# Performance work log

Measured on AMD Instinct MI355X. Metric: run time of the kernel, lower is better.

Reference implementation:

```python
import jax, jax.numpy as jnp
import numpy as np

MG = (5, 5)          # mesh_grid_size
UP = (17, 17)        # upsample_size
IMG = (512.0, 512.0) # image_size
B = 8192
FC_OUT = MG[0] * MG[1] * 2  # 50
KH = (UP[0] - 1) // (MG[0] - 1) + 1  # 5
KW = (UP[1] - 1) // (MG[1] - 1) + 1  # 5
SH = (UP[0] - 1) // (MG[0] - 1)      # 4
SW = (UP[1] - 1) // (MG[1] - 1)      # 4
L0 = MG[0] - 1
L1 = MG[1] - 1


def _grid(h, w):
    # channel 0: x coords vary along rows (image_size[0]); channel 1: y along cols
    x_t = jnp.broadcast_to(jnp.linspace(0.0, IMG[0], h)[:, None], (h, w))
    y_t = jnp.broadcast_to(jnp.linspace(0.0, IMG[1], w)[None, :], (h, w))
    return jnp.stack([x_t, y_t], 0)  # [2, h, w]


def _unfold22(a):
    # a: [B, 2, H, W] -> [B, (H-1)*(W-1), 4, 2]; 4 = kernel positions row-major, 2 = channel
    p = jnp.stack([a[:, :, :-1, :-1], a[:, :, :-1, 1:],
                   a[:, :, 1:, :-1], a[:, :, 1:, 1:]], axis=2)  # [B,2,4,H-1,W-1]
    return p.reshape(a.shape[0], 2, 4, -1).transpose(0, 3, 2, 1)


def _persp(src, dst):
    # exact 4-point homography solve (torchgeometry.get_perspective_transform)
    x0, y0 = src[..., 0], src[..., 1]
    u, v = dst[..., 0], dst[..., 1]
    z = jnp.zeros_like(x0)
    o = jnp.ones_like(x0)
    ax = jnp.stack([x0, y0, o, z, z, z, -u * x0, -u * y0], -1)  # [N,4,8]
    ay = jnp.stack([z, z, z, x0, y0, o, -v * x0, -v * y0], -1)
    A = jnp.concatenate([ax, ay], 1)                 # [N,8,8]
    bb = jnp.concatenate([u, v], 1)[..., None]       # [N,8,1]
    h = jnp.linalg.solve(A, bb)[..., 0]              # [N,8]
    return jnp.concatenate([h, o[:, :1]], 1).reshape(-1, 3, 3)


def setup_inputs() -> dict:
    key = jax.random.key(0)
    ks = jax.random.split(key, 4)
    def lin(k, i, o):
        return jax.random.normal(k, (i, o), jnp.float32) / jnp.sqrt(i)
    return {
        "x": jax.random.normal(ks[0], (B, 1024), jnp.float32),
        "W1": lin(ks[1], 1024, 1024), "b1": jnp.zeros((1024,), jnp.float32),
        "W2": lin(ks[2], 1024, 2048), "b2": jnp.zeros((2048,), jnp.float32),
        "W3": lin(ks[3], 2048, FC_OUT), "b3": jnp.zeros((FC_OUT,), jnp.float32),
    }


def reference(x, W1, b1, W2, b2, W3, b3):
    Bn = x.shape[0]
    h = jax.nn.relu(x @ W1 + b1)
    h = jax.nn.relu(h @ W2 + b2)
    out = (h @ W3 + b3).reshape(Bn, 2, MG[0], MG[1])  # [B,2,5,5] mesh flow

    # sparse control grid and 2x2 patch corner points
    gs = _grid(MG[0], MG[1])
    src = _unfold22(jnp.broadcast_to(gs[None], (Bn, 2, MG[0], MG[1]))).reshape(-1, 4, 2)
    flow = _unfold22(out).reshape(-1, 4, 2)
    M = _persp(src, src + flow)  # [B*16, 3, 3]

    # dense grid and its unfold2 (kernel KHxKW, stride SHxSW) patch points
    gd = _grid(UP[0], UP[1])  # [2, 17, 17]
    gi = (np.arange(L0) * SH)[:, None, None, None] + np.arange(KH)[None, None, :, None]
    gj = (np.arange(L1) * SW)[None, :, None, None] + np.arange(KW)[None, None, None, :]
    I, J = np.broadcast_arrays(gi, gj)  # [L0,L1,KH,KW]
    pts = gd[:, I, J].transpose(1, 2, 3, 4, 0).reshape(1, L0 * L1, KH * KW, 2)
    pts = jnp.broadcast_to(pts, (Bn, L0 * L1, KH * KW, 2)).reshape(Bn * L0 * L1, KH * KW, 2)

    # transform_points: homogeneous warp + perspective divide
    ph = jnp.concatenate([pts, jnp.ones(pts.shape[:-1] + (1,), pts.dtype)], -1)
    oh = jnp.einsum('nij,npj->npi', M, ph)
    warped = oh[..., :2] / oh[..., 2:3]
    warped = warped.reshape(Bn, L0, L1, KH, KW, 2)

    # Fold: scatter-accumulate overlapping patches
    fold = jnp.zeros((Bn, 2, UP[0], UP[1]), x.dtype)
    for i in range(L0):
        for j in range(L1):
            blk = warped[:, i, j].transpose(0, 3, 1, 2)  # [B,2,KH,KW]
            fold = fold.at[:, :, i * SH:i * SH + KH, j * SW:j * SW + KW].add(blk)

    # boundary rescaling exactly as the torch code: only the 5x5 crossing points
    idx = np.arange(0, UP[0], MG[0] - 1)
    X, Y = np.meshgrid(idx, idx, indexing='xy')
    fold = fold.at[:, :, X, Y].multiply(0.5)
    for (a, b) in ((0, 0), (0, UP[1] - 1), (UP[0] - 1, UP[1] - 1), (UP[0] - 1, 0)):
        fold = fold.at[:, :, a, b].multiply(2.0)

    return fold - gd[None]  # upsampled mesh flow [B,2,17,17]
```

## Files before the change

### kernel.cpp

```cpp
#include <hip/hip_runtime.h>

typedef __bf16 bf16x8 __attribute__((ext_vector_type(8)));
typedef float f32x4 __attribute__((ext_vector_type(4)));

__device__ __forceinline__ unsigned short f2bf(float f) {
  unsigned int u = __builtin_bit_cast(unsigned int, f);
  unsigned int r = (u + 0x7fffu + ((u >> 16) & 1u)) >> 16;
  return (unsigned short)r;
}

__device__ __forceinline__ float bf2f(unsigned short u) {
  unsigned int v = ((unsigned int)u) << 16;
  return __builtin_bit_cast(float, v);
}

__device__ __forceinline__ void load16_lds(const unsigned short* g, unsigned short* l) {
  __builtin_amdgcn_global_load_lds(
      (const __attribute__((address_space(1))) void*)g,
      (__attribute__((address_space(3))) void*)l, 16, 0, 0);
}

__device__ __forceinline__ void wait_vm0() {
  asm volatile("s_waitcnt vmcnt(0)" ::: "memory");
  __builtin_amdgcn_sched_barrier(0);
}
__device__ __forceinline__ void barrier_raw() {
  __builtin_amdgcn_sched_barrier(0);
  __builtin_amdgcn_s_barrier();
  __builtin_amdgcn_sched_barrier(0);
}


__global__ __launch_bounds__(256) void prepass(
    const float* __restrict__ x, const float* __restrict__ W1,
    const float* __restrict__ W2, const float* __restrict__ W3,
    unsigned short* __restrict__ xbf, unsigned short* __restrict__ w1t,
    unsigned short* __restrict__ w2t, unsigned short* __restrict__ w3t) {
  __shared__ float tile[32][33];
  const int bid = blockIdx.x;
  const int t = threadIdx.x;
  if (bid < 2048) {
    for (int i = bid * 256 + t; i < 2097152; i += 2048 * 256) {
      float4 f = ((const float4*)x)[i];
      uint2 o;
      o.x = (unsigned)f2bf(f.x) | ((unsigned)f2bf(f.y) << 16);
      o.y = (unsigned)f2bf(f.z) | ((unsigned)f2bf(f.w) << 16);
      ((uint2*)xbf)[i] = o;
    }
  } else if (bid < 3072) {
    int ti = bid - 2048;
    int n0 = (ti & 31) * 32, k0 = (ti >> 5) * 32;
    int tx = t & 31, ty = t >> 5;
    #pragma unroll
    for (int r = 0; r < 32; r += 8)
      tile[ty + r][tx] = W1[(size_t)(k0 + ty + r) * 1024 + n0 + tx];
    __syncthreads();
    #pragma unroll
    for (int r = 0; r < 32; r += 8)
      w1t[(size_t)(n0 + ty + r) * 1024 + k0 + tx] = f2bf(tile[tx][ty + r]);
  } else if (bid < 5120) {
    int ti = bid - 3072;
    int n0 = (ti & 63) * 32, k0 = (ti >> 6) * 32;
    int tx = t & 31, ty = t >> 5;
    #pragma unroll
    for (int r = 0; r < 32; r += 8)
      tile[ty + r][tx] = W2[(size_t)(k0 + ty + r) * 2048 + n0 + tx];
    __syncthreads();
    #pragma unroll
    for (int r = 0; r < 32; r += 8)
      w2t[(size_t)(n0 + ty + r) * 1024 + k0 + tx] = f2bf(tile[tx][ty + r]);
  } else {
    int idx = (bid - 5120) * 256 + t;
    int n = idx >> 11, k = idx & 2047;
    w3t[idx] = f2bf((n < 50) ? W3[(size_t)k * 50 + n] : 0.f);
  }
}


__global__ __launch_bounds__(512, 2) void gemm1_8p(
    const unsigned short* __restrict__ A,
    const unsigned short* __restrict__ Bt,
    const float* __restrict__ bias,
    unsigned short* __restrict__ C) {
  constexpr int K = 1024, N = 1024, NT = 16;
  constexpr int AEL = 256 * 64;
  constexpr int BEL = 128 * 64;
  constexpr int BUF = AEL + BEL;
  __shared__ __align__(16) unsigned short smem[2 * BUF];
  const int t = threadIdx.x;
  const int m0 = blockIdx.x * 256;
  const int n0 = blockIdx.y * 128;
  const int lane = t & 63, wv = t >> 6;
  const int l16 = lane & 15, quad = lane >> 4;
  const int rb = (wv >> 1) * 64, cb = (wv & 1) * 64;

  const int srow = t >> 3;
  const int sg = ((t & 7) ^ (srow & 7)) * 8;
  const unsigned short* Ag0 = A + (size_t)(m0 + srow) * K + sg;
  const unsigned short* Bg0 = Bt + (size_t)(n0 + srow) * K + sg;
  const int ldsO = wv * 8 * 64;

  f32x4 acc[4][4] = {};

  #pragma unroll
  for (int r = 0; r < 4; ++r)
    load16_lds(Ag0 + (size_t)(r * 64) * K, &smem[r * 4096 + ldsO]);
  #pragma unroll
  for (int r = 0; r < 2; ++r)
    load16_lds(Bg0 + (size_t)(r * 64) * K, &smem[AEL + r * 4096 + ldsO]);

  for (int kt = 0; kt < NT; ++kt) {
    unsigned short* Ls = &smem[(kt & 1) * BUF];

    wait_vm0();
    barrier_raw();

    if (kt + 1 < NT) {
      unsigned short* Ln = &smem[((kt + 1) & 1) * BUF];
      const unsigned short* An = Ag0 + (size_t)(kt + 1) * 64;
      const unsigned short* Bn = Bg0 + (size_t)(kt + 1) * 64;
      #pragma unroll
      for (int r = 0; r < 4; ++r)
        load16_lds(An + (size_t)(r * 64) * K, &Ln[r * 4096 + ldsO]);
      #pragma unroll
      for (int r = 0; r < 2; ++r)
        load16_lds(Bn + (size_t)(r * 64) * K, &Ln[AEL + r * 4096 + ldsO]);
    }

    #pragma unroll
    for (int half = 0; half < 2; ++half) {
      bf16x8 af[4], bfr[4];
      #pragma unroll
      for (int ni = 0; ni < 4; ++ni) {
        int row = cb + ni * 16 + l16;
        bfr[ni] = *(const bf16x8*)&Ls[AEL + row * 64 + ((half * 4 + quad) ^ (row & 7)) * 8];
      }
      #pragma unroll
      for (int mi = 0; mi < 4; ++mi) {
        int row = rb + mi * 16 + l16;
        af[mi] = *(const bf16x8*)&Ls[row * 64 + ((half * 4 + quad) ^ (row & 7)) * 8];
      }
      #pragma unroll
      for (int mi = 0; mi < 4; ++mi)
        #pragma unroll
        for (int ni = 0; ni < 4; ++ni)
          acc[mi][ni] = __builtin_amdgcn_mfma_f32_16x16x32_bf16(
              af[mi], bfr[ni], acc[mi][ni], 0, 0, 0);
    }
  }
  barrier_raw();

  unsigned short* Cs = smem;
  float bv[4];
  #pragma unroll
  for (int ni = 0; ni < 4; ++ni) bv[ni] = bias[n0 + cb + ni * 16 + l16];
  #pragma unroll
  for (int mi = 0; mi < 4; ++mi)
    #pragma unroll
    for (int ni = 0; ni < 4; ++ni)
      #pragma unroll
      for (int r = 0; r < 4; ++r) {
        int row = rb + mi * 16 + quad * 4 + r;
        int col = cb + ni * 16 + l16;
        int pb = (col >> 3) ^ (row & 15);
        Cs[row * 128 + pb * 8 + (col & 7)] = f2bf(fmaxf(acc[mi][ni][r] + bv[ni], 0.f));
      }
  __syncthreads();
  #pragma unroll
  for (int j = 0; j < 8; ++j) {
    int idx = j * 512 + t;
    int row = idx >> 4, cg = idx & 15;
    int pb = cg ^ (row & 15);
    *(uint4*)&C[(size_t)(m0 + row) * N + n0 + cg * 8] =
        *(const uint4*)&Cs[row * 128 + pb * 8];
  }
}


__global__ __launch_bounds__(512, 2) void gemm2_8p(
    const unsigned short* __restrict__ A,
    const unsigned short* __restrict__ Bt,
    const float* __restrict__ bias,
    const unsigned short* __restrict__ W3t,
    unsigned short* __restrict__ part) {
  constexpr int K = 1024, NT = 16;
  constexpr int AEL = 256 * 64;
  constexpr int BUF = 2 * AEL;
  __shared__ __align__(16) unsigned short smem[2 * BUF];
  const int t = threadIdx.x;
  const int m0 = blockIdx.x * 256;
  const int n0 = blockIdx.y * 256;
  const int lane = t & 63, wv = t >> 6;
  const int l16 = lane & 15, quad = lane >> 4;
  const int rb = (wv >> 2) * 128, cb = (wv & 3) * 64;

  const int srow = t >> 3;
  const int sg = ((t & 7) ^ (srow & 7)) * 8;
  const unsigned short* Ag0 = A + (size_t)(m0 + srow) * K + sg;
  const unsigned short* Bg0 = Bt + (size_t)(n0 + srow) * K + sg;
  const int ldsO = wv * 8 * 64;

  f32x4 acc[8][4] = {};

  #pragma unroll
  for (int r = 0; r < 4; ++r) {
    load16_lds(Ag0 + (size_t)(r * 64) * K, &smem[r * 4096 + ldsO]);
    load16_lds(Bg0 + (size_t)(r * 64) * K, &smem[AEL + r * 4096 + ldsO]);
  }

  for (int kt = 0; kt < NT; ++kt) {
    unsigned short* Ls = &smem[(kt & 1) * BUF];

    wait_vm0();
    barrier_raw();

    if (kt + 1 < NT) {
      unsigned short* Ln = &smem[((kt + 1) & 1) * BUF];
      const unsigned short* An = Ag0 + (size_t)(kt + 1) * 64;
      const unsigned short* Bn = Bg0 + (size_t)(kt + 1) * 64;
      #pragma unroll
      for (int r = 0; r < 4; ++r) {
        load16_lds(An + (size_t)(r * 64) * K, &Ln[r * 4096 + ldsO]);
        load16_lds(Bn + (size_t)(r * 64) * K, &Ln[AEL + r * 4096 + ldsO]);
      }
    }

    #pragma unroll
    for (int half = 0; half < 2; ++half) {
      bf16x8 bfr[4];
      #pragma unroll
      for (int ni = 0; ni < 4; ++ni) {
        int row = cb + ni * 16 + l16;
        bfr[ni] = *(const bf16x8*)&Ls[AEL + row * 64 + ((half * 4 + quad) ^ (row & 7)) * 8];
      }
      bf16x8 af[8];
      #pragma unroll
      for (int mi = 0; mi < 8; ++mi) {
        int row = rb + mi * 16 + l16;
        af[mi] = *(const bf16x8*)&Ls[row * 64 + ((half * 4 + quad) ^ (row & 7)) * 8];
      }
      #pragma unroll
      for (int mi = 0; mi < 8; ++mi)
        #pragma unroll
        for (int ni = 0; ni < 4; ++ni)
          acc[mi][ni] = __builtin_amdgcn_mfma_f32_16x16x32_bf16(
              af[mi], bfr[ni], acc[mi][ni], 0, 0, 0);
    }
  }
  barrier_raw();

  unsigned short* Cs = smem;
  float bv[4];
  #pragma unroll
  for (int ni = 0; ni < 4; ++ni) bv[ni] = bias[n0 + cb + ni * 16 + l16];
  #pragma unroll
  for (int mi = 0; mi < 8; ++mi)
    #pragma unroll
    for (int ni = 0; ni < 4; ++ni)
      #pragma unroll
      for (int r = 0; r < 4; ++r) {
        int row = rb + mi * 16 + quad * 4 + r;
        int col = cb + ni * 16 + l16;
        int pb = (col >> 3) ^ (row & 31);
        Cs[row * 256 + pb * 8 + (col & 7)] = f2bf(fmaxf(acc[mi][ni][r] + bv[ni], 0.f));
      }
  __syncthreads();

  bf16x8 bq[8][4];
  #pragma unroll
  for (int ks = 0; ks < 8; ++ks)
    #pragma unroll
    for (int nt = 0; nt < 4; ++nt)
      bq[ks][nt] = *(const bf16x8*)&W3t[(size_t)(nt * 16 + l16) * 2048 +
                                        n0 + ks * 32 + quad * 8];
  f32x4 acc2[2][4] = {};
  #pragma unroll
  for (int ks = 0; ks < 8; ++ks) {
    bf16x8 af2[2];
    #pragma unroll
    for (int mt = 0; mt < 2; ++mt) {
      int row = wv * 32 + mt * 16 + l16;
      int pb = (ks * 4 + quad) ^ (row & 31);
      af2[mt] = *(const bf16x8*)&Cs[row * 256 + pb * 8];
    }
    #pragma unroll
    for (int mt = 0; mt < 2; ++mt)
      #pragma unroll
      for (int nt = 0; nt < 4; ++nt)
        acc2[mt][nt] = __builtin_amdgcn_mfma_f32_16x16x32_bf16(
            af2[mt], bq[ks][nt], acc2[mt][nt], 0, 0, 0);
  }

  const int zi = blockIdx.y;
  #pragma unroll
  for (int mt = 0; mt < 2; ++mt)
    #pragma unroll
    for (int nt = 0; nt < 4; ++nt) {
      int col = nt * 16 + l16;
      #pragma unroll
      for (int r = 0; r < 4; ++r) {
        int row = m0 + wv * 32 + mt * 16 + quad * 4 + r;
        part[((size_t)row * 8 + zi) * 64 + col] = f2bf(acc2[mt][nt][r]);
      }
    }
}


__global__ __launch_bounds__(256) void geom_reduce(
    const unsigned short* __restrict__ part,
    const float* __restrict__ b3,
    float* __restrict__ outp) {
  __shared__ float s_out3[16 * 64];
  __shared__ float unfold[16][16][50];
  const int t = threadIdx.x;
  const int bbase = blockIdx.x * 16;

  for (int i = t; i < 1024; i += 256) {
    int m = i >> 6, n = i & 63;
    const unsigned short* p = part + ((size_t)(bbase + m) * 8) * 64 + n;
    float v = 0.f;
    #pragma unroll
    for (int z = 0; z < 8; ++z) v += bf2f(p[z * 64]);
    s_out3[i] = v + ((n < 50) ? b3[n] : 0.f);
  }
  __syncthreads();

  {
    const int bl = t >> 4;
    const int p = t & 15;
    const int pi = p >> 2, pj = p & 3;
    const float* o = &s_out3[bl * 64];

    float u00 = 128.f * pi       + o[pi * 5 + pj];
    float v00 = 128.f * pj       + o[25 + pi * 5 + pj];
    float u01 = 128.f * pi       + o[pi * 5 + pj + 1];
    float v01 = 128.f * (pj + 1) + o[25 + pi * 5 + pj + 1];
    float u10 = 128.f * (pi + 1) + o[(pi + 1) * 5 + pj];
    float v10 = 128.f * pj       + o[25 + (pi + 1) * 5 + pj];
    float u11 = 128.f * (pi + 1) + o[(pi + 1) * 5 + pj + 1];
    float v11 = 128.f * (pj + 1) + o[25 + (pi + 1) * 5 + pj + 1];

    float sx = u00 - u10 + u11 - u01;
    float sy = v00 - v10 + v11 - v01;
    float dx1 = u10 - u11, dx2 = u01 - u11;
    float dy1 = v10 - v11, dy2 = v01 - v11;
    float rden = 1.f / (dx1 * dy2 - dx2 * dy1);
    float g = (sx * dy2 - dx2 * sy) * rden;
    float h = (dx1 * sy - sx * dy1) * rden;
    float a = u10 - u00 + g * u10;
    float b = u01 - u00 + h * u01;
    float c = u00;
    float d = v10 - v00 + g * v10;
    float e = v01 - v00 + h * v01;
    float f = v00;

    #pragma unroll
    for (int ai = 0; ai < 5; ++ai) {
      #pragma unroll
      for (int bi = 0; bi < 5; ++bi) {
        float s = 0.25f * ai, tt = 0.25f * bi;
        float rw = 1.f / (g * s + h * tt + 1.f);
        unfold[bl][p][ai * 5 + bi]      = (a * s + b * tt + c) * rw;
        unfold[bl][p][25 + ai * 5 + bi] = (d * s + e * tt + f) * rw;
      }
    }
  }
  __syncthreads();

  for (int i = t; i < 16 * 578; i += 256) {
    int blb = i / 578;
    int rem = i - blb * 578;
    int ch = rem / 289;
    int ij = rem - ch * 289;
    int gi = ij / 17, gj = ij - gi * 17;

    int pi0 = (gi == 16) ? 3 : (gi >> 2);
    int ai0 = gi - 4 * pi0;
    int ci = (((gi & 3) == 0) && gi != 0 && gi != 16) ? 2 : 1;
    int pj0 = (gj == 16) ? 3 : (gj >> 2);
    int bj0 = gj - 4 * pj0;
    int cj = (((gj & 3) == 0) && gj != 0 && gj != 16) ? 2 : 1;

    float val = 0.f;
    #pragma unroll
    for (int ii = 0; ii < 2; ++ii) {
      if (ii < ci) {
        int pi = pi0 - ii, ai = ii ? 4 : ai0;
        #pragma unroll
        for (int jj = 0; jj < 2; ++jj) {
          if (jj < cj) {
            int pj = pj0 - jj, bi = jj ? 4 : bj0;
            val += unfold[blb][pi * 4 + pj][ch * 25 + ai * 5 + bi];
          }
        }
      }
    }

    if (((gi & 3) == 0) && ((gj & 3) == 0)) val *= 0.5f;
    if ((gi == 0 || gi == 16) && (gj == 0 || gj == 16)) val *= 2.f;
    val -= (ch == 0) ? 32.f * gi : 32.f * gj;
    outp[(size_t)(bbase + blb) * 578 + rem] = val;
  }
}


extern "C" void kernel_launch(void* const* d_in, const int* in_sizes, int n_in,
                              void* d_out, int out_size, void* d_ws, size_t ws_size,
                              hipStream_t stream) {
  const float* x  = (const float*)d_in[0];
  const float* W1 = (const float*)d_in[1];
  const float* b1 = (const float*)d_in[2];
  const float* W2 = (const float*)d_in[3];
  const float* b2 = (const float*)d_in[4];
  const float* W3 = (const float*)d_in[5];
  const float* b3 = (const float*)d_in[6];
  float* outp = (float*)d_out;

  char* ws = (char*)d_ws;
  unsigned short* xbf = (unsigned short*)ws;
  unsigned short* w1t = (unsigned short*)(ws + (size_t)16 * 1024 * 1024);
  unsigned short* part = (unsigned short*)ws;
  unsigned short* w2t = (unsigned short*)(ws + (size_t)34 * 1024 * 1024);
  unsigned short* w3t = (unsigned short*)(ws + (size_t)38 * 1024 * 1024);
  unsigned short* h1  = (unsigned short*)(ws + (size_t)38 * 1024 * 1024 + 512 * 1024);

  prepass<<<5632, 256, 0, stream>>>(x, W1, W2, W3, xbf, w1t, w2t, w3t);

  gemm1_8p<<<dim3(32, 8), 512, 0, stream>>>(xbf, w1t, b1, h1);
  gemm2_8p<<<dim3(32, 8), 512, 0, stream>>>(h1, w2t, b2, w3t, part);
  geom_reduce<<<512, 256, 0, stream>>>(part, b3, outp);
}
```

Measured before the change: 177.0 us.

## Fuse prepass, both GEMMs and geometry stage into one cooperative persistent kernel

Result: slower. 453.1 us (+156.0%).

```diff
diff --git a/kernel.cpp b/kernel.cpp
--- a/kernel.cpp
+++ b/kernel.cpp
@@ -1,4 +1,7 @@
 #include <hip/hip_runtime.h>
+#include <hip/hip_cooperative_groups.h>
+
+namespace cg = cooperative_groups;
 
 typedef __bf16 bf16x8 __attribute__((ext_vector_type(8)));
 typedef float f32x4 __attribute__((ext_vector_type(4)));
@@ -31,375 +34,381 @@
 }
 
 
-__global__ __launch_bounds__(256) void prepass(
+__global__ __launch_bounds__(512, 1) void mega(
     const float* __restrict__ x, const float* __restrict__ W1,
-    const float* __restrict__ W2, const float* __restrict__ W3,
-    unsigned short* __restrict__ xbf, unsigned short* __restrict__ w1t,
-    unsigned short* __restrict__ w2t, unsigned short* __restrict__ w3t) {
-  __shared__ float tile[32][33];
+    const float* __restrict__ b1, const float* __restrict__ W2,
+    const float* __restrict__ b2, const float* __restrict__ W3,
+    const float* __restrict__ b3,
+    unsigned short* xbf, unsigned short* w1t,
+    unsigned short* __restrict__ w2t, unsigned short* __restrict__ w3t,
+    unsigned short* h1, unsigned short* part,
+    float* __restrict__ outp) {
+  __shared__ __align__(16) unsigned char ldsraw[131072];
+  cg::grid_group grid = cg::this_grid();
+  const int t = threadIdx.x;
   const int bid = blockIdx.x;
-  const int t = threadIdx.x;
-  if (bid < 2048) {
-    for (int i = bid * 256 + t; i < 2097152; i += 2048 * 256) {
+
+  {
+    for (int i = bid * 512 + t; i < 2097152; i += 256 * 512) {
       float4 f = ((const float4*)x)[i];
       uint2 o;
       o.x = (unsigned)f2bf(f.x) | ((unsigned)f2bf(f.y) << 16);
       o.y = (unsigned)f2bf(f.z) | ((unsigned)f2bf(f.w) << 16);
       ((uint2*)xbf)[i] = o;
     }
-  } else if (bid < 3072) {
-    int ti = bid - 2048;
-    int n0 = (ti & 31) * 32, k0 = (ti >> 5) * 32;
-    int tx = t & 31, ty = t >> 5;
-    #pragma unroll
-    for (int r = 0; r < 32; r += 8)
-      tile[ty + r][tx] = W1[(size_t)(k0 + ty + r) * 1024 + n0 + tx];
+    {
+      int idx = bid * 512 + t;
+      int n = idx >> 11, k = idx & 2047;
+      w3t[idx] = f2bf((n < 50) ? W3[(size_t)k * 50 + n] : 0.f);
+    }
+    float (*tl2)[32][33] = (float(*)[32][33])ldsraw;
+    const int th = t >> 8;
+    const int tl = t & 255;
+    const int tx = tl & 31, ty = tl >> 5;
+    #pragma unroll
+    for (int rep = 0; rep < 2; ++rep) {
+      int ti = bid * 4 + rep * 2 + th;
+      int n0 = (ti & 31) * 32, k0 = (ti >> 5) * 32;
+      #pragma unroll
+      for (int r = 0; r < 32; r += 8)
+        tl2[th][ty + r][tx] = W1[(size_t)(k0 + ty + r) * 1024 + n0 + tx];
+      __syncthreads();
+      #pragma unroll
+      for (int r = 0; r < 32; r += 8)
+        w1t[(size_t)(n0 + ty + r) * 1024 + k0 + tx] = f2bf(tl2[th][tx][ty + r]);
+      __syncthreads();
+    }
+    #pragma unroll
+    for (int rep = 0; rep < 4; ++rep) {
+      int ti = bid * 8 + rep * 2 + th;
+      int n0 = (ti & 63) * 32, k0 = (ti >> 6) * 32;
+      #pragma unroll
+      for (int r = 0; r < 32; r += 8)
+        tl2[th][ty + r][tx] = W2[(size_t)(k0 + ty + r) * 2048 + n0 + tx];
+      __syncthreads();
+      #pragma unroll
+      for (int r = 0; r < 32; r += 8)
+        w2t[(size_t)(n0 + ty + r) * 1024 + k0 + tx] = f2bf(tl2[th][tx][ty + r]);
+      __syncthreads();
+    }
+  }
+  __threadfence();
+  grid.sync();
+
+  {
+    constexpr int K = 1024, N = 1024, NT = 16;
+    constexpr int AEL = 256 * 64;
+    constexpr int BEL = 128 * 64;
+    constexpr int BUF = AEL + BEL;
+    unsigned short* smem = (unsigned short*)ldsraw;
+    const int m0 = (bid >> 3) * 256;
+    const int n0 = (bid & 7) * 128;
+    const int lane = t & 63, wv = t >> 6;
+    const int l16 = lane & 15, quad = lane >> 4;
+    const int rb = (wv >> 1) * 64, cb = (wv & 1) * 64;
+
+    const int srow = t >> 3;
+    const int sg = ((t & 7) ^ (srow & 7)) * 8;
+    const unsigned short* Ag0 = xbf + (size_t)(m0 + srow) * K + sg;
+    const unsigned short* Bg0 = w1t + (size_t)(n0 + srow) * K + sg;
+    const int ldsO = wv * 8 * 64;
+
+    f32x4 acc[4][4] = {};
+
+    #pragma unroll
+    for (int r = 0; r < 4; ++r)
+      load16_lds(Ag0 + (size_t)(r * 64) * K, &smem[r * 4096 + ldsO]);
+    #pragma unroll
+    for (int r = 0; r < 2; ++r)
+      load16_lds(Bg0 + (size_t)(r * 64) * K, &smem[AEL + r * 4096 + ldsO]);
+
+    for (int kt = 0; kt < NT; ++kt) {
+      unsigned short* Ls = &smem[(kt & 1) * BUF];
+
+      wait_vm0();
+      barrier_raw();
+
+      if (kt + 1 < NT) {
+        unsigned short* Ln = &smem[((kt + 1) & 1) * BUF];
+        const unsigned short* An = Ag0 + (size_t)(kt + 1) * 64;
+        const unsigned short* Bn = Bg0 + (size_t)(kt + 1) * 64;
+        #pragma unroll
+        for (int r = 0; r < 4; ++r)
+          load16_lds(An + (size_t)(r * 64) * K, &Ln[r * 4096 + ldsO]);
+        #pragma unroll
+        for (int r = 0; r < 2; ++r)
+          load16_lds(Bn + (size_t)(r * 64) * K, &Ln[AEL + r * 4096 + ldsO]);
+      }
+
+      #pragma unroll
+      for (int half = 0; half < 2; ++half) {
+        bf16x8 af[4], bfr[4];
+        #pragma unroll
+        for (int ni = 0; ni < 4; ++ni) {
+          int row = cb + ni * 16 + l16;
+          bfr[ni] = *(const bf16x8*)&Ls[AEL + row * 64 + ((half * 4 + quad) ^ (row & 7)) * 8];
+        }
+        #pragma unroll
+        for (int mi = 0; mi < 4; ++mi) {
+          int row = rb + mi * 16 + l16;
+          af[mi] = *(const bf16x8*)&Ls[row * 64 + ((half * 4 + quad) ^ (row & 7)) * 8];
+        }
+        #pragma unroll
+        for (int mi = 0; mi < 4; ++mi)
+          #pragma unroll
+          for (int ni = 0; ni < 4; ++ni)
+            acc[mi][ni] = __builtin_amdgcn_mfma_f32_16x16x32_bf16(
+                af[mi], bfr[ni], acc[mi][ni], 0, 0, 0);
+      }
+    }
+    barrier_raw();
+
+    unsigned short* Cs = smem;
+    float bv[4];
+    #pragma unroll
+    for (int ni = 0; ni < 4; ++ni) bv[ni] = b1[n0 + cb + ni * 16 + l16];
+    #pragma unroll
+    for (int mi = 0; mi < 4; ++mi)
+      #pragma unroll
+      for (int ni = 0; ni < 4; ++ni)
+        #pragma unroll
+        for (int r = 0; r < 4; ++r) {
+          int row = rb + mi * 16 + quad * 4 + r;
+          int col = cb + ni * 16 + l16;
+          int pb = (col >> 3) ^ (row & 15);
+          Cs[row * 128 + pb * 8 + (col & 7)] = f2bf(fmaxf(acc[mi][ni][r] + bv[ni], 0.f));
+        }
     __syncthreads();
     #pragma unroll
-    for (int r = 0; r < 32; r += 8)
-      w1t[(size_t)(n0 + ty + r) * 1024 + k0 + tx] = f2bf(tile[tx][ty + r]);
-  } else if (bid < 5120) {
-    int ti = bid - 3072;
-    int n0 = (ti & 63) * 32, k0 = (ti >> 6) * 32;
-    int tx = t & 31, ty = t >> 5;
-    #pragma unroll
-    for (int r = 0; r < 32; r += 8)
-      tile[ty + r][tx] = W2[(size_t)(k0 + ty + r) * 2048 + n0 + tx];
+    for (int j = 0; j < 8; ++j) {
+      int idx = j * 512 + t;
+      int row = idx >> 4, cg2 = idx & 15;
+      int pb = cg2 ^ (row & 15);
+      *(uint4*)&h1[(size_t)(m0 + row) * N + n0 + cg2 * 8] =
+          *(const uint4*)&Cs[row * 128 + pb * 8];
+    }
+  }
+  __threadfence();
+  grid.sync();
+
+  {
+    constexpr int K = 1024, NT = 16;
+    constexpr int AEL = 256 * 64;
+    constexpr int BUF = 2 * AEL;
+    unsigned short* smem = (unsigned short*)ldsraw;
+    const int m0 = (bid >> 3) * 256;
+    const int n0 = (bid & 7) * 256;
+    const int lane = t & 63, wv = t >> 6;
+    const int l16 = lane & 15, quad = lane >> 4;
+    const int rb = (wv >> 2) * 128, cb = (wv & 3) * 64;
+
+    const int srow = t >> 3;
+    const int sg = ((t & 7) ^ (srow & 7)) * 8;
+    const unsigned short* Ag0 = h1 + (size_t)(m0 + srow) * K + sg;
+    const unsigned short* Bg0 = w2t + (size_t)(n0 + srow) * K + sg;
+    const int ldsO = wv * 8 * 64;
+
+    f32x4 acc[8][4] = {};
+
+    #pragma unroll
+    for (int r = 0; r < 4; ++r) {
+      load16_lds(Ag0 + (size_t)(r * 64) * K, &smem[r * 4096 + ldsO]);
+      load16_lds(Bg0 + (size_t)(r * 64) * K, &smem[AEL + r * 4096 + ldsO]);
+    }
+
+    for (int kt = 0; kt < NT; ++kt) {
+      unsigned short* Ls = &smem[(kt & 1) * BUF];
+
+      wait_vm0();
+      barrier_raw();
+
+      if (kt + 1 < NT) {
+        unsigned short* Ln = &smem[((kt + 1) & 1) * BUF];
+        const unsigned short* An = Ag0 + (size_t)(kt + 1) * 64;
+        const unsigned short* Bn = Bg0 + (size_t)(kt + 1) * 64;
+        #pragma unroll
+        for (int r = 0; r < 4; ++r) {
+          load16_lds(An + (size_t)(r * 64) * K, &Ln[r * 4096 + ldsO]);
+          load16_lds(Bn + (size_t)(r * 64) * K, &Ln[AEL + r * 4096 + ldsO]);
+        }
+      }
+
+      #pragma unroll
+      for (int half = 0; half < 2; ++half) {
+        bf16x8 bfr[4];
+        #pragma unroll
+        for (int ni = 0; ni < 4; ++ni) {
+          int row = cb + ni * 16 + l16;
+          bfr[ni] = *(const bf16x8*)&Ls[AEL + row * 64 + ((half * 4 + quad) ^ (row & 7)) * 8];
+        }
+        bf16x8 af[8];
+        #pragma unroll
+        for (int mi = 0; mi < 8; ++mi) {
+          int row = rb + mi * 16 + l16;
+          af[mi] = *(const bf16x8*)&Ls[row * 64 + ((half * 4 + quad) ^ (row & 7)) * 8];
+        }
+        #pragma unroll
+        for (int mi = 0; mi < 8; ++mi)
+          #pragma unroll
+          for (int ni = 0; ni < 4; ++ni)
+            acc[mi][ni] = __builtin_amdgcn_mfma_f32_16x16x32_bf16(
+                af[mi], bfr[ni], acc[mi][ni], 0, 0, 0);
+      }
+    }
+    barrier_raw();
+
+    unsigned short* Cs = smem;
+    float bv[4];
+    #pragma unroll
+    for (int ni = 0; ni < 4; ++ni) bv[ni] = b2[n0 + cb + ni * 16 + l16];
+    #pragma unroll
+    for (int mi = 0; mi < 8; ++mi)
+      #pragma unroll
+      for (int ni = 0; ni < 4; ++ni)
+        #pragma unroll
+        for (int r = 0; r < 4; ++r) {
+          int row = rb + mi * 16 + quad * 4 + r;
+          int col = cb + ni * 16 + l16;
+          int pb = (col >> 3) ^ (row & 31);
+          Cs[row * 256 + pb * 8 + (col & 7)] = f2bf(fmaxf(acc[mi][ni][r] + bv[ni], 0.f));
+        }
     __syncthreads();
-    #pragma unroll
-    for (int r = 0; r < 32; r += 8)
-      w2t[(size_t)(n0 + ty + r) * 1024 + k0 + tx] = f2bf(tile[tx][ty + r]);
-  } else {
-    int idx = (bid - 5120) * 256 + t;
-    int n = idx >> 11, k = idx & 2047;
-    w3t[idx] = f2bf((n < 50) ? W3[(size_t)k * 50 + n] : 0.f);
+
+    bf16x8 bq[8][4];
+    #pragma unroll
+    for (int ks = 0; ks < 8; ++ks)
+      #pragma unroll
+      for (int nt = 0; nt < 4; ++nt)
+        bq[ks][nt] = *(const bf16x8*)&w3t[(size_t)(nt * 16 + l16) * 2048 +
+                                          n0 + ks * 32 + quad * 8];
+    f32x4 acc2[2][4] = {};
+    #pragma unroll
+    for (int ks = 0; ks < 8; ++ks) {
+      bf16x8 af2[2];
+      #pragma unroll
+      for (int mt = 0; mt < 2; ++mt) {
+        int row = wv * 32 + mt * 16 + l16;
+        int pb = (ks * 4 + quad) ^ (row & 31);
+        af2[mt] = *(const bf16x8*)&Cs[row * 256 + pb * 8];
+      }
+      #pragma unroll
+      for (int mt = 0; mt < 2; ++mt)
+        #pragma unroll
+        for (int nt = 0; nt < 4; ++nt)
+          acc2[mt][nt] = __builtin_amdgcn_mfma_f32_16x16x32_bf16(
+              af2[mt], bq[ks][nt], acc2[mt][nt], 0, 0, 0);
+    }
+
+    const int zi = bid & 7;
+    #pragma unroll
+    for (int mt = 0; mt < 2; ++mt)
+      #pragma unroll
+      for (int nt = 0; nt < 4; ++nt) {
+        int col = nt * 16 + l16;
+        #pragma unroll
+        for (int r = 0; r < 4; ++r) {
+          int row = m0 + wv * 32 + mt * 16 + quad * 4 + r;
+          part[((size_t)row * 8 + zi) * 64 + col] = f2bf(acc2[mt][nt][r]);
+        }
+      }
   }
-}
-
-
-__global__ __launch_bounds__(512, 2) void gemm1_8p(
-    const unsigned short* __restrict__ A,
-    const unsigned short* __restrict__ Bt,
-    const float* __restrict__ bias,
-    unsigned short* __restrict__ C) {
-  constexpr int K = 1024, N = 1024, NT = 16;
-  constexpr int AEL = 256 * 64;
-  constexpr int BEL = 128 * 64;
-  constexpr int BUF = AEL + BEL;
-  __shared__ __align__(16) unsigned short smem[2 * BUF];
-  const int t = threadIdx.x;
-  const int m0 = blockIdx.x * 256;
-  const int n0 = blockIdx.y * 128;
-  const int lane = t & 63, wv = t >> 6;
-  const int l16 = lane & 15, quad = lane >> 4;
-  const int rb = (wv >> 1) * 64, cb = (wv & 1) * 64;
-
-  const int srow = t >> 3;
-  const int sg = ((t & 7) ^ (srow & 7)) * 8;
-  const unsigned short* Ag0 = A + (size_t)(m0 + srow) * K + sg;
-  const unsigned short* Bg0 = Bt + (size_t)(n0 + srow) * K + sg;
-  const int ldsO = wv * 8 * 64;
-
-  f32x4 acc[4][4] = {};
-
-  #pragma unroll
-  for (int r = 0; r < 4; ++r)
-    load16_lds(Ag0 + (size_t)(r * 64) * K, &smem[r * 4096 + ldsO]);
-  #pragma unroll
-  for (int r = 0; r < 2; ++r)
-    load16_lds(Bg0 + (size_t)(r * 64) * K, &smem[AEL + r * 4096 + ldsO]);
-
-  for (int kt = 0; kt < NT; ++kt) {
-    unsigned short* Ls = &smem[(kt & 1) * BUF];
-
-    wait_vm0();
-    barrier_raw();
-
-    if (kt + 1 < NT) {
-      unsigned short* Ln = &smem[((kt + 1) & 1) * BUF];
-      const unsigned short* An = Ag0 + (size_t)(kt + 1) * 64;
-      const unsigned short* Bn = Bg0 + (size_t)(kt + 1) * 64;
-      #pragma unroll
-      for (int r = 0; r < 4; ++r)
-        load16_lds(An + (size_t)(r * 64) * K, &Ln[r * 4096 + ldsO]);
-      #pragma unroll
-      for (int r = 0; r < 2; ++r)
-        load16_lds(Bn + (size_t)(r * 64) * K, &Ln[AEL + r * 4096 + ldsO]);
-    }
-
-    #pragma unroll
-    for (int half = 0; half < 2; ++half) {
-      bf16x8 af[4], bfr[4];
-      #pragma unroll
-      for (int ni = 0; ni < 4; ++ni) {
-        int row = cb + ni * 16 + l16;
-        bfr[ni] = *(const bf16x8*)&Ls[AEL + row * 64 + ((half * 4 + quad) ^ (row & 7)) * 8];
-      }
-      #pragma unroll
-      for (int mi = 0; mi < 4; ++mi) {
-        int row = rb + mi * 16 + l16;
-        af[mi] = *(const bf16x8*)&Ls[row * 64 + ((half * 4 + quad) ^ (row & 7)) * 8];
-      }
-      #pragma unroll
-      for (int mi = 0; mi < 4; ++mi)
-        #pragma unroll
-        for (int ni = 0; ni < 4; ++ni)
-          acc[mi][ni] = __builtin_amdgcn_mfma_f32_16x16x32_bf16(
-              af[mi], bfr[ni], acc[mi][ni], 0, 0, 0);
-    }
-  }
-  barrier_raw();
-
-  unsigned short* Cs = smem;
-  float bv[4];
-  #pragma unroll
-  for (int ni = 0; ni < 4; ++ni) bv[ni] = bias[n0 + cb + ni * 16 + l16];
-  #pragma unroll
-  for (int mi = 0; mi < 4; ++mi)
-    #pragma unroll
-    for (int ni = 0; ni < 4; ++ni)
-      #pragma unroll
-      for (int r = 0; r < 4; ++r) {
-        int row = rb + mi * 16 + quad * 4 + r;
-        int col = cb + ni * 16 + l16;
-        int pb = (col >> 3) ^ (row & 15);
-        Cs[row * 128 + pb * 8 + (col & 7)] = f2bf(fmaxf(acc[mi][ni][r] + bv[ni], 0.f));
-      }
-  __syncthreads();
-  #pragma unroll
-  for (int j = 0; j < 8; ++j) {
-    int idx = j * 512 + t;
-    int row = idx >> 4, cg = idx & 15;
-    int pb = cg ^ (row & 15);
-    *(uint4*)&C[(size_t)(m0 + row) * N + n0 + cg * 8] =
-        *(const uint4*)&Cs[row * 128 + pb * 8];
-  }
-}
-
-
-__global__ __launch_bounds__(512, 2) void gemm2_8p(
-    const unsigned short* __restrict__ A,
-    const unsigned short* __restrict__ Bt,
-    const float* __restrict__ bias,
-    const unsigned short* __restrict__ W3t,
-    unsigned short* __restrict__ part) {
-  constexpr int K = 1024, NT = 16;
-  constexpr int AEL = 256 * 64;
-  constexpr int BUF = 2 * AEL;
-  __shared__ __align__(16) unsigned short smem[2 * BUF];
-  const int t = threadIdx.x;
-  const int m0 = blockIdx.x * 256;
-  const int n0 = blockIdx.y * 256;
-  const int lane = t & 63, wv = t >> 6;
-  const int l16 = lane & 15, quad = lane >> 4;
-  const int rb = (wv >> 2) * 128, cb = (wv & 3) * 64;
-
-  const int srow = t >> 3;
-  const int sg = ((t & 7) ^ (srow & 7)) * 8;
-  const unsigned short* Ag0 = A + (size_t)(m0 + srow) * K + sg;
-  const unsigned short* Bg0 = Bt + (size_t)(n0 + srow) * K + sg;
-  const int ldsO = wv * 8 * 64;
-
-  f32x4 acc[8][4] = {};
-
-  #pragma unroll
-  for (int r = 0; r < 4; ++r) {
-    load16_lds(Ag0 + (size_t)(r * 64) * K, &smem[r * 4096 + ldsO]);
-    load16_lds(Bg0 + (size_t)(r * 64) * K, &smem[AEL + r * 4096 + ldsO]);
-  }
-
-  for (int kt = 0; kt < NT; ++kt) {
-    unsigned short* Ls = &smem[(kt & 1) * BUF];
-
-    wait_vm0();
-    barrier_raw();
-
-    if (kt + 1 < NT) {
-      unsigned short* Ln = &smem[((kt + 1) & 1) * BUF];
-      const unsigned short* An = Ag0 + (size_t)(kt + 1) * 64;
-      const unsigned short* Bn = Bg0 + (size_t)(kt + 1) * 64;
-      #pragma unroll
-      for (int r = 0; r < 4; ++r) {
-        load16_lds(An + (size_t)(r * 64) * K, &Ln[r * 4096 + ldsO]);
-        load16_lds(Bn + (size_t)(r * 64) * K, &Ln[AEL + r * 4096 + ldsO]);
-      }
-    }
-
-    #pragma unroll
-    for (int half = 0; half < 2; ++half) {
-      bf16x8 bfr[4];
-      #pragma unroll
-      for (int ni = 0; ni < 4; ++ni) {
-        int row = cb + ni * 16 + l16;
-        bfr[ni] = *(const bf16x8*)&Ls[AEL + row * 64 + ((half * 4 + quad) ^ (row & 7)) * 8];
-      }
-      bf16x8 af[8];
-      #pragma unroll
-      for (int mi = 0; mi < 8; ++mi) {
-        int row = rb + mi * 16 + l16;
-        af[mi] = *(const bf16x8*)&Ls[row * 64 + ((half * 4 + quad) ^ (row & 7)) * 8];
-      }
-      #pragma unroll
-      for (int mi = 0; mi < 8; ++mi)
-        #pragma unroll
-        for (int ni = 0; ni < 4; ++ni)
-          acc[mi][ni] = __builtin_amdgcn_mfma_f32_16x16x32_bf16(
-              af[mi], bfr[ni], acc[mi][ni], 0, 0, 0);
-    }
-  }
-  barrier_raw();
-
-  unsigned short* Cs = smem;
-  float bv[4];
-  #pragma unroll
-  for (int ni = 0; ni < 4; ++ni) bv[ni] = bias[n0 + cb + ni * 16 + l16];
-  #pragma unroll
-  for (int mi = 0; mi < 8; ++mi)
-    #pragma unroll
-    for (int ni = 0; ni < 4; ++ni)
-      #pragma unroll
-      for (int r = 0; r < 4; ++r) {
-        int row = rb + mi * 16 + quad * 4 + r;
-        int col = cb + ni * 16 + l16;
-        int pb = (col >> 3) ^ (row & 31);
-        Cs[row * 256 + pb * 8 + (col & 7)] = f2bf(fmaxf(acc[mi][ni][r] + bv[ni], 0.f));
-      }
-  __syncthreads();
-
-  bf16x8 bq[8][4];
-  #pragma unroll
-  for (int ks = 0; ks < 8; ++ks)
-    #pragma unroll
-    for (int nt = 0; nt < 4; ++nt)
-      bq[ks][nt] = *(const bf16x8*)&W3t[(size_t)(nt * 16 + l16) * 2048 +
-                                        n0 + ks * 32 + quad * 8];
-  f32x4 acc2[2][4] = {};
-  #pragma unroll
-  for (int ks = 0; ks < 8; ++ks) {
-    bf16x8 af2[2];
-    #pragma unroll
-    for (int mt = 0; mt < 2; ++mt) {
-      int row = wv * 32 + mt * 16 + l16;
-      int pb = (ks * 4 + quad) ^ (row & 31);
-      af2[mt] = *(const bf16x8*)&Cs[row * 256 + pb * 8];
-    }
-    #pragma unroll
-    for (int mt = 0; mt < 2; ++mt)
-      #pragma unroll
-      for (int nt = 0; nt < 4; ++nt)
-        acc2[mt][nt] = __builtin_amdgcn_mfma_f32_16x16x32_bf16(
-            af2[mt], bq[ks][nt], acc2[mt][nt], 0, 0, 0);
-  }
-
-  const int zi = blockIdx.y;
-  #pragma unroll
-  for (int mt = 0; mt < 2; ++mt)
-    #pragma unroll
-    for (int nt = 0; nt < 4; ++nt) {
-      int col = nt * 16 + l16;
-      #pragma unroll
-      for (int r = 0; r < 4; ++r) {
-        int row = m0 + wv * 32 + mt * 16 + quad * 4 + r;
-        part[((size_t)row * 8 + zi) * 64 + col] = f2bf(acc2[mt][nt][r]);
-      }
-    }
-}
-
-
-__global__ __launch_bounds__(256) void geom_reduce(
-    const unsigned short* __restrict__ part,
-    const float* __restrict__ b3,
-    float* __restrict__ outp) {
-  __shared__ float s_out3[16 * 64];
-  __shared__ float unfold[16][16][50];
-  const int t = threadIdx.x;
-  const int bbase = blockIdx.x * 16;
-
-  for (int i = t; i < 1024; i += 256) {
-    int m = i >> 6, n = i & 63;
-    const unsigned short* p = part + ((size_t)(bbase + m) * 8) * 64 + n;
-    float v = 0.f;
-    #pragma unroll
-    for (int z = 0; z < 8; ++z) v += bf2f(p[z * 64]);
-    s_out3[i] = v + ((n < 50) ? b3[n] : 0.f);
-  }
-  __syncthreads();
+  __threadfence();
+  grid.sync();
 
   {
-    const int bl = t >> 4;
-    const int p = t & 15;
-    const int pi = p >> 2, pj = p & 3;
-    const float* o = &s_out3[bl * 64];
-
-    float u00 = 128.f * pi       + o[pi * 5 + pj];
-    float v00 = 128.f * pj       + o[25 + pi * 5 + pj];
-    float u01 = 128.f * pi       + o[pi * 5 + pj + 1];
-    float v01 = 128.f * (pj + 1) + o[25 + pi * 5 + pj + 1];
-    float u10 = 128.f * (pi + 1) + o[(pi + 1) * 5 + pj];
-    float v10 = 128.f * pj       + o[25 + (pi + 1) * 5 + pj];
-    float u11 = 128.f * (pi + 1) + o[(pi + 1) * 5 + pj + 1];
-    float v11 = 128.f * (pj + 1) + o[25 + (pi + 1) * 5 + pj + 1];
-
-    float sx = u00 - u10 + u11 - u01;
-    float sy = v00 - v10 + v11 - v01;
-    float dx1 = u10 - u11, dx2 = u01 - u11;
-    float dy1 = v10 - v11, dy2 = v01 - v11;
-    float rden = 1.f / (dx1 * dy2 - dx2 * dy1);
-    float g = (sx * dy2 - dx2 * sy) * rden;
-    float h = (dx1 * sy - sx * dy1) * rden;
-    float a = u10 - u00 + g * u10;
-    float b = u01 - u00 + h * u01;
-    float c = u00;
-    float d = v10 - v00 + g * v10;
-    float e = v01 - v00 + h * v01;
-    float f = v00;
-
-    #pragma unroll
-    for (int ai = 0; ai < 5; ++ai) {
-      #pragma unroll
-      for (int bi = 0; bi < 5; ++bi) {
-        float s = 0.25f * ai, tt = 0.25f * bi;
-        float rw = 1.f / (g * s + h * tt + 1.f);
-        unfold[bl][p][ai * 5 + bi]      = (a * s + b * tt + c) * rw;
-        unfold[bl][p][25 + ai * 5 + bi] = (d * s + e * tt + f) * rw;
-      }
-    }
-  }
-  __syncthreads();
-
-  for (int i = t; i < 16 * 578; i += 256) {
-    int blb = i / 578;
-    int rem = i - blb * 578;
-    int ch = rem / 289;
-    int ij = rem - ch * 289;
-    int gi = ij / 17, gj = ij - gi * 17;
-
-    int pi0 = (gi == 16) ? 3 : (gi >> 2);
-    int ai0 = gi - 4 * pi0;
-    int ci = (((gi & 3) == 0) && gi != 0 && gi != 16) ? 2 : 1;
-    int pj0 = (gj == 16) ? 3 : (gj >> 2);
-    int bj0 = gj - 4 * pj0;
-    int cj = (((gj & 3) == 0) && gj != 0 && gj != 16) ? 2 : 1;
-
-    float val = 0.f;
-    #pragma unroll
-    for (int ii = 0; ii < 2; ++ii) {
-      if (ii < ci) {
-        int pi = pi0 - ii, ai = ii ? 4 : ai0;
-        #pragma unroll
-        for (int jj = 0; jj < 2; ++jj) {
-          if (jj < cj) {
-            int pj = pj0 - jj, bi = jj ? 4 : bj0;
-            val += unfold[blb][pi * 4 + pj][ch * 25 + ai * 5 + bi];
+    const int half = t >> 8;
+    const int tl = t & 255;
+    const int bbase = (bid * 2 + half) * 16;
+    float* s_out3 = (float*)ldsraw + half * 1024;
+    float (*unfold)[16][50] =
+        ((float(*)[16][50])(ldsraw + 8192)) + (size_t)half * 16;
+
+    for (int i = tl; i < 1024; i += 256) {
+      int m = i >> 6, n = i & 63;
+      const unsigned short* p = part + ((size_t)(bbase + m) * 8) * 64 + n;
+      float v = 0.f;
+      #pragma unroll
+      for (int z = 0; z < 8; ++z) v += bf2f(p[z * 64]);
+      s_out3[i] = v + ((n < 50) ? b3[n] : 0.f);
+    }
+    __syncthreads();
+
+    {
+      const int bl = tl >> 4;
+      const int p = tl & 15;
+      const int pi = p >> 2, pj = p & 3;
+      const float* o = &s_out3[bl * 64];
+
+      float u00 = 128.f * pi       + o[pi * 5 + pj];
+      float v00 = 128.f * pj       + o[25 + pi * 5 + pj];
+      float u01 = 128.f * pi       + o[pi * 5 + pj + 1];
+      float v01 = 128.f * (pj + 1) + o[25 + pi * 5 + pj + 1];
+      float u10 = 128.f * (pi + 1) + o[(pi + 1) * 5 + pj];
+      float v10 = 128.f * pj       + o[25 + (pi + 1) * 5 + pj];
+      float u11 = 128.f * (pi + 1) + o[(pi + 1) * 5 + pj + 1];
+      float v11 = 128.f * (pj + 1) + o[25 + (pi + 1) * 5 + pj + 1];
+
+      float sx = u00 - u10 + u11 - u01;
+      float sy = v00 - v10 + v11 - v01;
+      float dx1 = u10 - u11, dx2 = u01 - u11;
+      float dy1 = v10 - v11, dy2 = v01 - v11;
+      float rden = 1.f / (dx1 * dy2 - dx2 * dy1);
+      float g = (sx * dy2 - dx2 * sy) * rden;
+      float h = (dx1 * sy - sx * dy1) * rden;
+      float a = u10 - u00 + g * u10;
+      float b = u01 - u00 + h * u01;
+      float c = u00;
+      float d = v10 - v00 + g * v10;
+      float e = v01 - v00 + h * v01;
+      float f = v00;
+
+      #pragma unroll
+      for (int ai = 0; ai < 5; ++ai) {
+        #pragma unroll
+        for (int bi = 0; bi < 5; ++bi) {
+          float s = 0.25f * ai, tt = 0.25f * bi;
+          float rw = 1.f / (g * s + h * tt + 1.f);
+          unfold[bl][p][ai * 5 + bi]      = (a * s + b * tt + c) * rw;
+          unfold[bl][p][25 + ai * 5 + bi] = (d * s + e * tt + f) * rw;
+        }
+      }
+    }
+    __syncthreads();
+
+    for (int i = tl; i < 16 * 578; i += 256) {
+      int blb = i / 578;
+      int rem = i - blb * 578;
+      int ch = rem / 289;
+      int ij = rem - ch * 289;
+      int gi = ij / 17, gj = ij - gi * 17;
+
+      int pi0 = (gi == 16) ? 3 : (gi >> 2);
+      int ai0 = gi - 4 * pi0;
+      int ci = (((gi & 3) == 0) && gi != 0 && gi != 16) ? 2 : 1;
+      int pj0 = (gj == 16) ? 3 : (gj >> 2);
+      int bj0 = gj - 4 * pj0;
+      int cj = (((gj & 3) == 0) && gj != 0 && gj != 16) ? 2 : 1;
+
+      float val = 0.f;
+      #pragma unroll
+      for (int ii = 0; ii < 2; ++ii) {
+        if (ii < ci) {
+          int pi = pi0 - ii, ai = ii ? 4 : ai0;
+          #pragma unroll
+          for (int jj = 0; jj < 2; ++jj) {
+            if (jj < cj) {
+              int pj = pj0 - jj, bi = jj ? 4 : bj0;
+              val += unfold[blb][pi * 4 + pj][ch * 25 + ai * 5 + bi];
+            }
           }
         }
       }
-    }
-
-    if (((gi & 3) == 0) && ((gj & 3) == 0)) val *= 0.5f;
-    if ((gi == 0 || gi == 16) && (gj == 0 || gj == 16)) val *= 2.f;
-    val -= (ch == 0) ? 32.f * gi : 32.f * gj;
-    outp[(size_t)(bbase + blb) * 578 + rem] = val;
+
+      if (((gi & 3) == 0) && ((gj & 3) == 0)) val *= 0.5f;
+      if ((gi == 0 || gi == 16) && (gj == 0 || gj == 16)) val *= 2.f;
+      val -= (ch == 0) ? 32.f * gi : 32.f * gj;
+      outp[(size_t)(bbase + blb) * 578 + rem] = val;
+    }
   }
 }
 
@@ -424,9 +433,10 @@
   unsigned short* w3t = (unsigned short*)(ws + (size_t)38 * 1024 * 1024);
   unsigned short* h1  = (unsigned short*)(ws + (size_t)38 * 1024 * 1024 + 512 * 1024);
 
-  prepass<<<5632, 256, 0, stream>>>(x, W1, W2, W3, xbf, w1t, w2t, w3t);
-
-  gemm1_8p<<<dim3(32, 8), 512, 0, stream>>>(xbf, w1t, b1, h1);
-  gemm2_8p<<<dim3(32, 8), 512, 0, stream>>>(h1, w2t, b2, w3t, part);
-  geom_reduce<<<512, 256, 0, stream>>>(part, b3, outp);
-}
+  void* args[] = {(void*)&x,   (void*)&W1,  (void*)&b1,  (void*)&W2,
+                  (void*)&b2,  (void*)&W3,  (void*)&b3,  (void*)&xbf,
+                  (void*)&w1t, (void*)&w2t, (void*)&w3t, (void*)&h1,
+                  (void*)&part, (void*)&outp};
+  hipLaunchCooperativeKernel((const void*)mega, dim3(256), dim3(512), args, 0,
+                             stream);
+}
```
